# Kernel optimization log

Measured on AMD Instinct MI355X. Metric: run time of the kernel, lower is better.

The kernel has to match this reference:

```python
import jax, jax.numpy as jnp
import numpy as np

N_WIRES = 8; N_LAYERS = 2; SEQ = 8; FEAT = 4; N_CLASS = 10
DIM = 2 ** N_WIRES; KEEP = N_WIRES - FEAT

# design: per layer, U3 on every wire then C(U3) ring (control q -> target (q+1)%n)
DESIGN = []
for l in range(N_LAYERS):
    for q in range(N_WIRES):
        DESIGN.append(('U3', (q,), l))
    for q in range(N_WIRES):
        DESIGN.append(('C(U3)', (q, (q + 1) % N_WIRES), l))

_idx = np.arange(DIM)
_bits = (_idx[:, None] >> np.arange(N_WIRES - 1, -1, -1)[None, :]) & 1  # wire 0 = MSB (kron order)
# hamming distance between basis indices -> weak-measurement dephasing on all wires
HDIST = jnp.asarray((_bits[:, None, :] ^ _bits[None, :, :]).sum(-1).astype(np.float32))
ZSIGN = jnp.asarray((1 - 2 * _bits.T).astype(np.float32))  # (n_wires, DIM): tr(rho Z_i) signs


def u3_mat(p):
    th, ph, lam = p[0], p[1], p[2]
    c = jnp.cos(th / 2).astype(jnp.complex64)
    s = jnp.sin(th / 2).astype(jnp.complex64)
    eip = jnp.exp(1j * ph).astype(jnp.complex64)
    eil = jnp.exp(1j * lam).astype(jnp.complex64)
    return jnp.stack([jnp.stack([c, -eil * s]), jnp.stack([eip * s, eip * eil * c])])


def cu3_mat(p):
    return jnp.eye(4, dtype=jnp.complex64).at[2:, 2:].set(u3_mat(p))


def apply_1q(rho, U, w):
    # rho' = U_w rho U_w^dagger on batched (B, DIM, DIM) density matrices
    rt = rho.reshape((-1,) + (2,) * (2 * N_WIRES))
    rt = jnp.moveaxis(jnp.tensordot(U, rt, axes=((1,), (1 + w,))), 0, 1 + w)
    rt = jnp.moveaxis(jnp.tensordot(jnp.conj(U), rt, axes=((1,), (1 + N_WIRES + w,))), 0, 1 + N_WIRES + w)
    return rt.reshape(rho.shape)


def apply_2q(rho, U4, c, t):
    Ur = U4.reshape(2, 2, 2, 2)  # (c', t', c, t)
    rt = rho.reshape((-1,) + (2,) * (2 * N_WIRES))
    rt = jnp.moveaxis(jnp.tensordot(Ur, rt, axes=((2, 3), (1 + c, 1 + t))), (0, 1), (1 + c, 1 + t))
    o = 1 + N_WIRES
    rt = jnp.moveaxis(jnp.tensordot(jnp.conj(Ur), rt, axes=((2, 3), (o + c, o + t))), (0, 1), (o + c, o + t))
    return rt.reshape(rho.shape)


def bkron(A, B):
    b, a = A.shape[0], A.shape[1]
    d = B.shape[-1]
    return jnp.einsum('bij,bkl->bikjl', A, B).reshape(b, a * d, a * d)


def x_to_rho_batch(xv):
    # xv: (B, F) in [0,1] -> (B, 2^F, 2^F); fold matches torch: rho = kron(rho_i, rho)
    s = jnp.sqrt((1.0 - xv) * xv)
    r = jnp.stack([jnp.stack([1.0 - xv, s], -1), jnp.stack([s, xv], -1)], -2).astype(jnp.complex64)
    rho = r[:, 0]
    for i in range(1, xv.shape[1]):
        rho = bkron(r[:, i], rho)
    return rho


def _forward(x, q_rot, q_ent, g_raw, fc_w, fc_b):
    g = jax.nn.softplus(g_raw)
    deph = jnp.exp(-(g * g) / 2.0 * HDIST).astype(jnp.complex64)
    B = x.shape[0]
    rho0 = jnp.zeros((DIM, DIM), jnp.complex64).at[0, 0].set(1.0)  # |0...0><0...0|
    rho = jnp.tile(rho0[None], (B, 1, 1))

    def body(rho, x_t):
        # partial trace over the FEAT most-significant qubits
        rt = rho.reshape(B, 2 ** FEAT, 2 ** KEEP, 2 ** FEAT, 2 ** KEEP)
        red = jnp.einsum('bijik->bjk', rt)
        rho = bkron(red, x_to_rho_batch(x_t))  # kron(kept, input)
        for op, wires, layer in DESIGN:
            if op == 'U3':
                rho = apply_1q(rho, u3_mat(q_rot[layer, wires[0]]), wires[0])
            else:
                rho = apply_2q(rho, cu3_mat(q_ent[layer, wires[0]]), wires[0], wires[1])
        rho = rho * deph  # weak measurement dephasing on every wire
        diag = jnp.real(jnp.einsum('bii->bi', rho))
        return rho, jnp.einsum('ba,ia->bi', diag, ZSIGN)  # <Z_i> per wire

    _, exps = jax.lax.scan(jax.checkpoint(body), rho, jnp.swapaxes(x, 0, 1))
    feats = jnp.transpose(exps, (1, 0, 2)).reshape(B, SEQ * N_WIRES)
    return feats @ fc_w.T + fc_b


def setup_inputs() -> dict:
    key = jax.random.key(0)
    ks = jax.random.split(key, 5)
    B = 64
    x = jax.random.uniform(ks[0], (B, SEQ, FEAT), jnp.float32)
    q_rot = np.float32(np.pi) * jax.random.uniform(ks[1], (N_LAYERS, N_WIRES, 3), jnp.float32)
    q_ent = np.float32(np.pi) * jax.random.uniform(ks[2], (N_LAYERS, N_WIRES, 3), jnp.float32)
    g_raw = jnp.float32(np.log(np.exp(1.0) - 1.0))  # softplus^{-1}(1)
    fc_w = 0.1 * jax.random.normal(ks[3], (N_CLASS, SEQ * N_WIRES), jnp.float32)
    fc_b = jnp.zeros((N_CLASS,), jnp.float32)
    return {"x": x, "q_params_rot": q_rot, "q_params_enta": q_ent, "g_raw": g_raw, "fc_w": fc_w, "fc_b": fc_b}


def reference(x, q_params_rot, q_params_enta, g_raw, fc_w, fc_b):
    return _forward(x, q_params_rot, q_params_enta, g_raw, fc_w, fc_b)
```

## Files before the change

### kernel.cpp

```cpp
#include <hip/hip_runtime.h>
#include <math.h>

#define SEQ 8
#define NCLASS 10

typedef float v2f __attribute__((ext_vector_type(2)));

__device__ __forceinline__ v2f pkfma(v2f a, v2f b, v2f c) {
    return __builtin_elementwise_fma(a, b, c);
}

__device__ inline float2 cmul(float2 a, float2 b) {
    return make_float2(a.x * b.x - a.y * b.y, a.x * b.y + a.y * b.x);
}

__device__ __forceinline__ void gload_lds16(const float4* g, float4* l) {
    __builtin_amdgcn_global_load_lds(
        (const __attribute__((address_space(1))) void*)g,
        (__attribute__((address_space(3))) void*)l, 16, 0, 0);
}

__global__ __launch_bounds__(256) void build_w_kernel(
    const float* __restrict__ qrot, const float* __restrict__ qent,
    float2* __restrict__ WT) {
    __shared__ float4 US[32][2];
    __shared__ int    metaS[32];
    const int t = threadIdx.x;
    if (t < 32) {
        const int l = t >> 4, wi = t & 15;
        int bc = -1, qt;
        const float* p;
        if (wi < 8) { qt = wi; p = qrot + (l * 8 + wi) * 3; }
        else { const int qc = wi - 8; qt = (qc + 1) & 7; p = qent + (l * 8 + qc) * 3; bc = 7 - qc; }
        const float th = p[0], ph = p[1], lam = p[2];
        const float c = cosf(0.5f * th), s = sinf(0.5f * th);
        US[t][0] = make_float4(c, 0.0f, -cosf(lam) * s, -sinf(lam) * s);
        US[t][1] = make_float4(cosf(ph) * s, sinf(ph) * s,
                               cosf(ph + lam) * c, sinf(ph + lam) * c);
        metaS[t] = ((bc + 1) << 8) | (7 - qt);
    }
    __syncthreads();

    const int lane = t & 63;
    const int col = blockIdx.x * 4 + (t >> 6);
    const int rbase = lane * 4;
    float2 a[4];
#pragma unroll
    for (int i = 0; i < 4; ++i)
        a[i] = make_float2((rbase + i) == col ? 1.0f : 0.0f, 0.0f);

    for (int g = 0; g < 32; ++g) {
        const int meta = metaS[g];
        const int bt = meta & 255;
        const int bcp1 = meta >> 8;
        const float4 u0 = US[g][0];
        const float4 u1 = US[g][1];
        const float2 U00 = make_float2(u0.x, u0.y);
        const float2 U01 = make_float2(u0.z, u0.w);
        const float2 U10 = make_float2(u1.x, u1.y);
        const float2 U11 = make_float2(u1.z, u1.w);
        const int mt = 1 << bt;
        if (bt >= 2) {
            const int pl = mt >> 2;
            const int side = (lane >> (bt - 2)) & 1;
            float2 br[4];
#pragma unroll
            for (int i = 0; i < 4; ++i) {
                br[i].x = __shfl_xor(a[i].x, pl, 64);
                br[i].y = __shfl_xor(a[i].y, pl, 64);
            }
#pragma unroll
            for (int i = 0; i < 4; ++i) {
                const int r = rbase + i;
                float2 na, tt;
                if (side) { na = cmul(U10, br[i]); tt = cmul(U11, a[i]); }
                else      { na = cmul(U00, a[i]); tt = cmul(U01, br[i]); }
                na.x += tt.x; na.y += tt.y;
                const bool act = (bcp1 == 0) || ((r >> (bcp1 - 1)) & 1);
                if (act) a[i] = na;
            }
        } else {
#pragma unroll
            for (int i0 = 0; i0 < 4; ++i0) {
                if (i0 & mt) continue;
                const int i1 = i0 | mt;
                const int r0 = rbase + i0;
                const bool act = (bcp1 == 0) || ((r0 >> (bcp1 - 1)) & 1);
                const float2 a0 = a[i0], a1 = a[i1];
                float2 n0 = cmul(U00, a0), t1 = cmul(U01, a1);
                n0.x += t1.x; n0.y += t1.y;
                float2 n1 = cmul(U10, a0), t2 = cmul(U11, a1);
                n1.x += t2.x; n1.y += t2.y;
                if (act) { a[i0] = n0; a[i1] = n1; }
            }
        }
    }
    float4* dst = (float4*)&WT[col * 256 + rbase];
    dst[0] = make_float4(a[0].x, a[0].y, a[1].x, a[1].y);
    dst[1] = make_float4(a[2].x, a[2].y, a[3].x, a[3].y);
}

__global__ __launch_bounds__(256) void wv_kernel(
    const float* __restrict__ x, const float2* __restrict__ WT,
    float4* __restrict__ WvT4) {
    __shared__ float w16s[16];
    __shared__ float2 sS[256][17];
    const int tid = threadIdx.x;
    const int b = blockIdx.x & 63;
    const int t = blockIdx.x >> 6;
    if (tid < 16) {
        float prod = 1.0f;
#pragma unroll
        for (int i = 0; i < 4; ++i) {
            const float xv = x[(b * SEQ + t) * 4 + i];
            prod *= ((tid >> i) & 1) ? sqrtf(xv) : sqrtf(1.0f - xv);
        }
        w16s[tid] = prod;
    }
    __syncthreads();
    float w16[16];
#pragma unroll
    for (int k = 0; k < 16; ++k) w16[k] = w16s[k];
    const float2* wrow = WT + tid;
#pragma unroll
    for (int j = 0; j < 16; ++j) {
        float2 acc = make_float2(0.0f, 0.0f);
#pragma unroll
        for (int k = 0; k < 16; ++k) {
            const float2 wv = wrow[(j * 16 + k) * 256];
            acc.x = fmaf(wv.x, w16[k], acc.x);
            acc.y = fmaf(wv.y, w16[k], acc.y);
        }
        sS[tid][j] = acc;
    }
    __syncthreads();
    float4* dst = WvT4 + (t * 64 + b) * 2048;
#pragma unroll
    for (int s = 0; s < 8; ++s) {
        const int e0 = 2 * tid + 512 * s;
        const int I0 = e0 >> 4, j0 = e0 & 15;
        const int u = j0 >> 1;
        const float2 a = sS[I0][j0];
        const float2 c = sS[I0][j0 + 1];
        dst[(I0 << 3) | (u ^ (I0 & 7))] = make_float4(a.x, a.y, c.x, c.y);
    }
}

__global__ __launch_bounds__(1024)
__attribute__((amdgpu_waves_per_eu(4, 4)))
void evolve_kernel(
    const float* __restrict__ g_raw_p,
    const float* __restrict__ fc_w, const float* __restrict__ fc_b,
    const float4* __restrict__ WvT4, float* __restrict__ out) {
    __shared__ float4 WvS4[2][16][16][8];
    __shared__ float4 SSp4[16][16][8];
    __shared__ float2 redS[16][16];
    __shared__ float dvalS[256];
    __shared__ float dephS[8];
    __shared__ float featsS[64];

    const int tid = threadIdx.x;
    const int b = blockIdx.x;
    const int f = tid >> 6;
    const int lane = tid & 63;
    const int r = lane >> 2;
    const int g = lane & 3;
    const int rs = r & 7;

    if (tid < 256) redS[tid >> 4][tid & 15] = make_float2(tid == 0 ? 1.0f : 0.0f, 0.0f);
    const float gg = log1pf(expf(g_raw_p[0]));
    if (tid < 8) dephS[tid] = expf(-0.5f * gg * gg * (float)tid);

    {
        const float4* src = WvT4 + b * 2048 + f * 128;
        gload_lds16(src + lane, &WvS4[0][f][0][0]);
        gload_lds16(src + 64 + lane, &WvS4[0][f][8][0]);
    }
    __syncthreads();

    for (int t = 0; t < SEQ; ++t) {
        const int buf = t & 1;
        if (t + 1 < SEQ) {
            const float4* src = WvT4 + ((t + 1) * 64 + b) * 2048 + f * 128;
            gload_lds16(src + lane, &WvS4[buf ^ 1][f][0][0]);
            gload_lds16(src + 64 + lane, &WvS4[buf ^ 1][f][8][0]);
        }

        v2f A0 = {0,0}, A1 = {0,0}, A2 = {0,0}, A3 = {0,0};
        v2f B0 = {0,0}, B1 = {0,0}, B2 = {0,0}, B3 = {0,0};
#pragma unroll
        for (int u = 0; u < 8; ++u) {
            const float4 wv = WvS4[buf][f][r][u ^ rs];
            const float4 ra = *(const float4*)&redS[2 * u][4 * g];
            const float4 rb = *(const float4*)&redS[2 * u][4 * g + 2];
            const float4 rc = *(const float4*)&redS[2 * u + 1][4 * g];
            const float4 rd = *(const float4*)&redS[2 * u + 1][4 * g + 2];
            const v2f wx = {wv.x, wv.x}, wy = {wv.y, wv.y};
            const v2f wz = {wv.z, wv.z}, ww = {wv.w, wv.w};
            const v2f ra0 = {ra.x, ra.y}, ra1 = {ra.z, ra.w};
            const v2f rb0 = {rb.x, rb.y}, rb1 = {rb.z, rb.w};
            const v2f rc0 = {rc.x, rc.y}, rc1 = {rc.z, rc.w};
            const v2f rd0 = {rd.x, rd.y}, rd1 = {rd.z, rd.w};
            A0 = pkfma(wx, ra0, A0);  B0 = pkfma(wy, ra0, B0);
            A1 = pkfma(wx, ra1, A1);  B1 = pkfma(wy, ra1, B1);
            A2 = pkfma(wx, rb0, A2);  B2 = pkfma(wy, rb0, B2);
            A3 = pkfma(wx, rb1, A3);  B3 = pkfma(wy, rb1, B3);
            A0 = pkfma(wz, rc0, A0);  B0 = pkfma(ww, rc0, B0);
            A1 = pkfma(wz, rc1, A1);  B1 = pkfma(ww, rc1, B1);
            A2 = pkfma(wz, rd0, A2);  B2 = pkfma(ww, rd0, B2);
            A3 = pkfma(wz, rd1, A3);  B3 = pkfma(ww, rd1, B3);
        }
        const v2f h0 = {A0.x - B0.y, A0.y + B0.x};
        const v2f h1 = {A1.x - B1.y, A1.y + B1.x};
        const v2f h2 = {A2.x - B2.y, A2.y + B2.x};
        const v2f h3 = {A3.x - B3.y, A3.y + B3.x};

        float2 s4[4];
#pragma unroll
        for (int pr = 0; pr < 4; ++pr) {
            float2 qq[2];
#pragma unroll
            for (int hh = 0; hh < 2; ++hh) {
                const int i = pr + 4 * hh;
                const int ms = i & 7;
                const float4 waA = WvS4[buf][f][i][(2 * g) ^ ms];
                const float4 wbA = WvS4[buf][f][i][(2 * g + 1) ^ ms];
                v2f PA = {0,0}, PB = {0,0};
                PA = pkfma((v2f){waA.x, waA.x}, h0, PA);  PB = pkfma((v2f){waA.y, waA.y}, h0, PB);
                PA = pkfma((v2f){waA.z, waA.z}, h1, PA);  PB = pkfma((v2f){waA.w, waA.w}, h1, PB);
                PA = pkfma((v2f){wbA.x, wbA.x}, h2, PA);  PB = pkfma((v2f){wbA.y, wbA.y}, h2, PB);
                PA = pkfma((v2f){wbA.z, wbA.z}, h3, PA);  PB = pkfma((v2f){wbA.w, wbA.w}, h3, PB);
                const float2 pa = make_float2(PA.x + PB.y, PA.y - PB.x);
                const float4 waB = WvS4[buf][f][i + 8][(2 * g) ^ ms];
                const float4 wbB = WvS4[buf][f][i + 8][(2 * g + 1) ^ ms];
                v2f QA = {0,0}, QB = {0,0};
                QA = pkfma((v2f){waB.x, waB.x}, h0, QA);  QB = pkfma((v2f){waB.y, waB.y}, h0, QB);
                QA = pkfma((v2f){waB.z, waB.z}, h1, QA);  QB = pkfma((v2f){waB.w, waB.w}, h1, QB);
                QA = pkfma((v2f){wbB.x, wbB.x}, h2, QA);  QB = pkfma((v2f){wbB.y, wbB.y}, h2, QB);
                QA = pkfma((v2f){wbB.z, wbB.z}, h3, QA);  QB = pkfma((v2f){wbB.w, wbB.w}, h3, QB);
                const float2 pb = make_float2(QA.x + QB.y, QA.y - QB.x);
                const float sx = (g & 1) ? pa.x : pb.x;
                const float sy = (g & 1) ? pa.y : pb.y;
                const float rx = __shfl_xor(sx, 1, 64);
                const float ry = __shfl_xor(sy, 1, 64);
                const float kx = (g & 1) ? pb.x : pa.x;
                const float ky = (g & 1) ? pb.y : pa.y;
                qq[hh] = make_float2(kx + rx, ky + ry);
            }
            const float sx = (g & 2) ? qq[0].x : qq[1].x;
            const float sy = (g & 2) ? qq[0].y : qq[1].y;
            const float rx = __shfl_xor(sx, 2, 64);
            const float ry = __shfl_xor(sy, 2, 64);
            const float kx = (g & 2) ? qq[1].x : qq[0].x;
            const float ky = (g & 2) ? qq[1].y : qq[0].y;
            s4[pr] = make_float2(kx + rx, ky + ry);
        }
        const int mpbase = 8 * (g & 1) + 4 * ((g >> 1) & 1);

        {
            const int u0 = mpbase >> 1;
            SSp4[f][r][u0 ^ rs]       = make_float4(s4[0].x, s4[0].y, s4[1].x, s4[1].y);
            SSp4[f][r][(u0 + 1) ^ rs] = make_float4(s4[2].x, s4[2].y, s4[3].x, s4[3].y);
        }
        {
            const int Q = r >> 2;
            const int gh = ((Q & 1) << 1) | (Q >> 1);
            if (g == gh) {
                float dv = s4[0].x;
                if ((r & 3) == 1) dv = s4[1].x;
                if ((r & 3) == 2) dv = s4[2].x;
                if ((r & 3) == 3) dv = s4[3].x;
                dvalS[f * 16 + r] = dv;
            }
        }
        __syncthreads();

        if (tid < 256) {
            const int m = tid >> 4, mp = tid & 15;
            const float2* S2 = (const float2*)SSp4;
            v2f sv = {0.0f, 0.0f};
            const int ci = mp ^ ((m & 7) * 2);
#pragma unroll
            for (int ff = 0; ff < 16; ++ff) {
                const float2 v = S2[(ff * 16 + m) * 16 + ci];
                sv += (v2f){v.x, v.y};
            }
            const float dp = dephS[__popc(m ^ mp)];
            redS[m][mp] = make_float2(sv.x * dp, sv.y * dp);
        } else if (f >= 8) {
            const int w = f - 8;
            const float4 dv = ((const float4*)dvalS)[lane];
            float v = 0.0f;
#pragma unroll
            for (int i = 0; i < 4; ++i) {
                const int d = 4 * lane + i;
                const float val = (i == 0) ? dv.x : (i == 1) ? dv.y : (i == 2) ? dv.z : dv.w;
                v += ((d >> (7 - w)) & 1) ? -val : val;
            }
#pragma unroll
            for (int off = 32; off >= 1; off >>= 1) v += __shfl_xor(v, off, 64);
            if (lane == 0) featsS[t * 8 + w] = v;
        }
        __syncthreads();
    }

    if (tid < NCLASS) {
        float acc = fc_b[tid];
#pragma unroll
        for (int qq = 0; qq < 64; ++qq)
            acc = fmaf(featsS[qq], fc_w[tid * 64 + qq], acc);
        out[b * NCLASS + tid] = acc;
    }
}

extern "C" void kernel_launch(void* const* d_in, const int* in_sizes, int n_in,
                              void* d_out, int out_size, void* d_ws, size_t ws_size,
                              hipStream_t stream) {
    (void)in_sizes; (void)n_in; (void)out_size; (void)ws_size;
    const float* x    = (const float*)d_in[0];
    const float* qrot = (const float*)d_in[1];
    const float* qent = (const float*)d_in[2];
    const float* graw = (const float*)d_in[3];
    const float* fcw  = (const float*)d_in[4];
    const float* fcb  = (const float*)d_in[5];
    float* out = (float*)d_out;

    float2* WT  = (float2*)d_ws;
    float4* WvT = (float4*)((char*)d_ws + 524288);

    build_w_kernel<<<64, 256, 0, stream>>>(qrot, qent, WT);
    wv_kernel<<<512, 256, 0, stream>>>(x, WT, WvT);
    evolve_kernel<<<64, 1024, 0, stream>>>(graw, fcw, fcb, WvT, out);
}
```

Baseline: 85.43 us.

## Fuse Wv projection into evolve kernel and drop separate wv kernel

Removes the intermediate wv_kernel launch and its 8MB-scale workspace round trip. The build kernel now writes the circuit unitary in a row-major float4 layout. Each evolve block computes its per-timestep W·v product on the fly from that unitary and the input amplitudes, writing straight into the double-buffered LDS tile. Next-step products are computed after the barrier, so they overlap with the reduction phase. The cost is that every block rereads the 256x256 unitary from global/L2 at each step and does the extra FMAs inside the serial loop.

Measured after the change: 177.9 us. +108.3%, slower.

```diff
diff --git a/kernel.cpp b/kernel.cpp
--- a/kernel.cpp
+++ b/kernel.cpp
@@ -14,17 +14,12 @@
     return make_float2(a.x * b.x - a.y * b.y, a.x * b.y + a.y * b.x);
 }
 
-__device__ __forceinline__ void gload_lds16(const float4* g, float4* l) {
-    __builtin_amdgcn_global_load_lds(
-        (const __attribute__((address_space(1))) void*)g,
-        (__attribute__((address_space(3))) void*)l, 16, 0, 0);
-}
-
 __global__ __launch_bounds__(256) void build_w_kernel(
     const float* __restrict__ qrot, const float* __restrict__ qent,
-    float2* __restrict__ WT) {
+    float4* __restrict__ Wr4) {
     __shared__ float4 US[32][2];
     __shared__ int    metaS[32];
+    __shared__ float2 colS[4][256];
     const int t = threadIdx.x;
     if (t < 32) {
         const int l = t >> 4, wi = t & 15;
@@ -42,7 +37,8 @@
     __syncthreads();
 
     const int lane = t & 63;
-    const int col = blockIdx.x * 4 + (t >> 6);
+    const int wid = t >> 6;
+    const int col = blockIdx.x * 4 + wid;
     const int rbase = lane * 4;
     float2 a[4];
 #pragma unroll
@@ -95,69 +91,57 @@
             }
         }
     }
-    float4* dst = (float4*)&WT[col * 256 + rbase];
-    dst[0] = make_float4(a[0].x, a[0].y, a[1].x, a[1].y);
-    dst[1] = make_float4(a[2].x, a[2].y, a[3].x, a[3].y);
-}
-
-__global__ __launch_bounds__(256) void wv_kernel(
-    const float* __restrict__ x, const float2* __restrict__ WT,
-    float4* __restrict__ WvT4) {
-    __shared__ float w16s[16];
-    __shared__ float2 sS[256][17];
-    const int tid = threadIdx.x;
-    const int b = blockIdx.x & 63;
-    const int t = blockIdx.x >> 6;
-    if (tid < 16) {
-        float prod = 1.0f;
-#pragma unroll
-        for (int i = 0; i < 4; ++i) {
-            const float xv = x[(b * SEQ + t) * 4 + i];
-            prod *= ((tid >> i) & 1) ? sqrtf(xv) : sqrtf(1.0f - xv);
-        }
-        w16s[tid] = prod;
-    }
+#pragma unroll
+    for (int i = 0; i < 4; ++i) colS[wid][rbase + i] = a[i];
     __syncthreads();
-    float w16[16];
-#pragma unroll
-    for (int k = 0; k < 16; ++k) w16[k] = w16s[k];
-    const float2* wrow = WT + tid;
-#pragma unroll
-    for (int j = 0; j < 16; ++j) {
-        float2 acc = make_float2(0.0f, 0.0f);
-#pragma unroll
-        for (int k = 0; k < 16; ++k) {
-            const float2 wv = wrow[(j * 16 + k) * 256];
-            acc.x = fmaf(wv.x, w16[k], acc.x);
-            acc.y = fmaf(wv.y, w16[k], acc.y);
-        }
-        sS[tid][j] = acc;
-    }
-    __syncthreads();
-    float4* dst = WvT4 + (t * 64 + b) * 2048;
-#pragma unroll
-    for (int s = 0; s < 8; ++s) {
-        const int e0 = 2 * tid + 512 * s;
-        const int I0 = e0 >> 4, j0 = e0 & 15;
-        const int u = j0 >> 1;
-        const float2 a = sS[I0][j0];
-        const float2 c = sS[I0][j0 + 1];
-        dst[(I0 << 3) | (u ^ (I0 & 7))] = make_float4(a.x, a.y, c.x, c.y);
-    }
+    const int u0 = blockIdx.x * 2;
+    const float2 c0 = colS[0][t], c1 = colS[1][t], c2 = colS[2][t], c3 = colS[3][t];
+    Wr4[t * 128 + u0]     = make_float4(c0.x, c0.y, c1.x, c1.y);
+    Wr4[t * 128 + u0 + 1] = make_float4(c2.x, c2.y, c3.x, c3.y);
+}
+
+__device__ __forceinline__ void compute_wv_piece(
+    const float4* __restrict__ wr,
+    const float* __restrict__ w16row,
+    float4* __restrict__ dst0,
+    float4* __restrict__ dst1) {
+    v2f w2[8];
+    const float4* wp = (const float4*)w16row;
+#pragma unroll
+    for (int i = 0; i < 4; ++i) {
+        const float4 v = wp[i];
+        w2[2 * i]     = (v2f){v.x, v.y};
+        w2[2 * i + 1] = (v2f){v.z, v.w};
+    }
+    v2f acc0 = {0,0}, acc1 = {0,0}, acc2 = {0,0}, acc3 = {0,0};
+#pragma unroll
+    for (int s = 0; s < 32; ++s) {
+        const float4 Wc = wr[s];
+        const v2f wk = w2[s & 7];
+        const v2f k0 = {wk.x, wk.x}, k1 = {wk.y, wk.y};
+        const v2f wa = {Wc.x, Wc.y}, wb = {Wc.z, Wc.w};
+        if ((s >> 3) == 0) { acc0 = pkfma(wa, k0, acc0); acc0 = pkfma(wb, k1, acc0); }
+        if ((s >> 3) == 1) { acc1 = pkfma(wa, k0, acc1); acc1 = pkfma(wb, k1, acc1); }
+        if ((s >> 3) == 2) { acc2 = pkfma(wa, k0, acc2); acc2 = pkfma(wb, k1, acc2); }
+        if ((s >> 3) == 3) { acc3 = pkfma(wa, k0, acc3); acc3 = pkfma(wb, k1, acc3); }
+    }
+    *dst0 = make_float4(acc0.x, acc0.y, acc1.x, acc1.y);
+    *dst1 = make_float4(acc2.x, acc2.y, acc3.x, acc3.y);
 }
 
 __global__ __launch_bounds__(1024)
 __attribute__((amdgpu_waves_per_eu(4, 4)))
 void evolve_kernel(
-    const float* __restrict__ g_raw_p,
+    const float* __restrict__ x, const float* __restrict__ g_raw_p,
     const float* __restrict__ fc_w, const float* __restrict__ fc_b,
-    const float4* __restrict__ WvT4, float* __restrict__ out) {
+    const float4* __restrict__ Wr4, float* __restrict__ out) {
     __shared__ float4 WvS4[2][16][16][8];
     __shared__ float4 SSp4[16][16][8];
     __shared__ float2 redS[16][16];
     __shared__ float dvalS[256];
     __shared__ float dephS[8];
     __shared__ float featsS[64];
+    __shared__ float w16S[SEQ][16];
 
     const int tid = threadIdx.x;
     const int b = blockIdx.x;
@@ -170,21 +154,26 @@
     if (tid < 256) redS[tid >> 4][tid & 15] = make_float2(tid == 0 ? 1.0f : 0.0f, 0.0f);
     const float gg = log1pf(expf(g_raw_p[0]));
     if (tid < 8) dephS[tid] = expf(-0.5f * gg * gg * (float)tid);
-
-    {
-        const float4* src = WvT4 + b * 2048 + f * 128;
-        gload_lds16(src + lane, &WvS4[0][f][0][0]);
-        gload_lds16(src + 64 + lane, &WvS4[0][f][8][0]);
-    }
+    if (tid < 128) {
+        const int tt = tid >> 4, k = tid & 15;
+        float prod = 1.0f;
+#pragma unroll
+        for (int i = 0; i < 4; ++i) {
+            const float xv = x[(b * SEQ + tt) * 4 + i];
+            prod *= ((k >> i) & 1) ? sqrtf(xv) : sqrtf(1.0f - xv);
+        }
+        w16S[tt][k] = prod;
+    }
+    __syncthreads();
+
+    const float4* wrBase = Wr4 + (16 * f + r) * 128 + 32 * g;
+
+    compute_wv_piece(wrBase, &w16S[0][0],
+                     &WvS4[0][f][r][(2 * g) ^ rs], &WvS4[0][f][r][(2 * g + 1) ^ rs]);
     __syncthreads();
 
     for (int t = 0; t < SEQ; ++t) {
         const int buf = t & 1;
-        if (t + 1 < SEQ) {
-            const float4* src = WvT4 + ((t + 1) * 64 + b) * 2048 + f * 128;
-            gload_lds16(src + lane, &WvS4[buf ^ 1][f][0][0]);
-            gload_lds16(src + 64 + lane, &WvS4[buf ^ 1][f][8][0]);
-        }
 
         v2f A0 = {0,0}, A1 = {0,0}, A2 = {0,0}, A3 = {0,0};
         v2f B0 = {0,0}, B1 = {0,0}, B2 = {0,0}, B3 = {0,0};
@@ -275,6 +264,12 @@
         }
         __syncthreads();
 
+        if (t + 1 < SEQ) {
+            const int nbuf = buf ^ 1;
+            compute_wv_piece(wrBase, &w16S[t + 1][0],
+                             &WvS4[nbuf][f][r][(2 * g) ^ rs],
+                             &WvS4[nbuf][f][r][(2 * g + 1) ^ rs]);
+        }
         if (tid < 256) {
             const int m = tid >> 4, mp = tid & 15;
             const float2* S2 = (const float2*)SSp4;
@@ -325,10 +320,8 @@
     const float* fcb  = (const float*)d_in[5];
     float* out = (float*)d_out;
 
-    float2* WT  = (float2*)d_ws;
-    float4* WvT = (float4*)((char*)d_ws + 524288);
-
-    build_w_kernel<<<64, 256, 0, stream>>>(qrot, qent, WT);
-    wv_kernel<<<512, 256, 0, stream>>>(x, WT, WvT);
-    evolve_kernel<<<64, 1024, 0, stream>>>(graw, fcw, fcb, WvT, out);
-}
+    float4* Wr4 = (float4*)d_ws;
+
+    build_w_kernel<<<64, 256, 0, stream>>>(qrot, qent, Wr4);
+    evolve_kernel<<<64, 1024, 0, stream>>>(x, graw, fcw, fcb, Wr4, out);
+}
```
